# Kernel optimization log

Hardware: AMD Instinct MI355X
Metric: run time of the kernel (lower is better)

## Reference

```python
import jax, jax.numpy as jnp
import numpy as np

M = 0.25      # margin m
GAMMA = 64.0  # scale gamma
N, D = 8192, 128
NUM_CLASSES = 512


def setup_inputs() -> dict:
    key = jax.random.key(0)
    k1, k2 = jax.random.split(key)
    inputs = jax.random.normal(k1, (N, D), dtype=jnp.float32)
    targets = jax.random.randint(k2, (N,), 0, NUM_CLASSES, dtype=jnp.int64)
    return {"inputs": inputs, "targets": targets}


def reference(inputs, targets):
    # L2-normalize rows -> cosine similarity matrix [n, n]
    x = inputs / jnp.linalg.norm(inputs, axis=1, keepdims=True)
    sim = x @ x.T
    # positive mask: same label (includes diagonal, matching the torch code)
    mask = targets[:, None] == targets[None, :]

    Op, On = 1.0 + M, -M
    delta_p, delta_n = 1.0 - M, M

    sim_d = jax.lax.stop_gradient(sim)  # .detach() in torch
    ap = jnp.maximum(Op - sim_d, 0.0)
    an = jnp.maximum(sim_d + On, 0.0)

    logit_p = -ap * (sim - delta_p) * GAMMA
    logit_n = an * (sim - delta_n) * GAMMA

    neg_inf = jnp.float32(-jnp.inf)
    # per-row logsumexp over positives of -logit_p, over negatives of logit_n
    lp = jax.nn.logsumexp(jnp.where(mask, -logit_p, neg_inf), axis=1)
    ln = jax.nn.logsumexp(jnp.where(mask, neg_inf, logit_n), axis=1)

    return jnp.mean(jax.nn.softplus(ln + lp))
```

## Files before the change

### kernel.cpp

```cpp
#include <hip/hip_runtime.h>
#include <math.h>


#define NR    8192
#define DIMK  128
#define NT    64
#define NBLKS 512

typedef __attribute__((ext_vector_type(8))) short short8;
typedef __attribute__((ext_vector_type(4))) float f32x4;
typedef __attribute__((address_space(3))) uint32_t lds_u32;
typedef const __attribute__((address_space(1))) uint32_t glb_u32;

__device__ __forceinline__ unsigned short bf16_rne(float f) {
  uint32_t u = __float_as_uint(f);
  u += 0x7FFFu + ((u >> 16) & 1u);
  return (unsigned short)(u >> 16);
}


__global__ __launch_bounds__(256) void normalize_split_kernel(
    const float* __restrict__ x, unsigned short* __restrict__ xhi,
    unsigned short* __restrict__ xlo, float* __restrict__ gP,
    float* __restrict__ gN, int* __restrict__ counter) {
  if (blockIdx.x < 32)      gP[blockIdx.x * 256 + threadIdx.x] = 0.f;
  else if (blockIdx.x < 64) gN[(blockIdx.x - 32) * 256 + threadIdx.x] = 0.f;
  if (blockIdx.x == 64 && threadIdx.x == 0) *counter = 0;

  const int wave = threadIdx.x >> 6;
  const int lane = threadIdx.x & 63;
  const int row  = blockIdx.x * 4 + wave;
  const float2 v = ((const float2*)(x + (size_t)row * DIMK))[lane];
  float ss = v.x * v.x + v.y * v.y;
  #pragma unroll
  for (int s = 1; s < 64; s <<= 1) ss += __shfl_xor(ss, s);
  const float r = rsqrtf(ss);
  const float a = v.x * r, b = v.y * r;
  const unsigned short ha = bf16_rne(a), hb = bf16_rne(b);
  const float haf = __uint_as_float((uint32_t)ha << 16);
  const float hbf = __uint_as_float((uint32_t)hb << 16);
  ushort2 hi, lo;
  hi.x = ha; hi.y = hb;
  lo.x = bf16_rne(a - haf); lo.y = bf16_rne(b - hbf);
  ((ushort2*)xhi)[(size_t)row * 64 + lane] = hi;
  ((ushort2*)xlo)[(size_t)row * 64 + lane] = lo;
}

__global__ __launch_bounds__(512, 2) void simloss_kernel(
    const unsigned short* __restrict__ xhi, const unsigned short* __restrict__ xlo,
    const int* __restrict__ tgt, float* __restrict__ gP, float* __restrict__ gN,
    int* __restrict__ counter, float* __restrict__ out) {
  __shared__ unsigned short S[32768];
  __shared__ float colbuf[2][4][128][2];
  __shared__ int tAs[2][128];
  __shared__ int tBs[5][128];
  __shared__ float red[512];
  __shared__ int islast;

  const int tid  = threadIdx.x;
  const int wave = tid >> 6, lane = tid & 63;
  const int wy = wave & 3, wx = wave >> 2;
  const int q = lane >> 4, mcol = lane & 15;
  const bool isStage = (wy == 1) || (wy == 2);
  const bool isFlush = (wy == 0);
  const int srank = (wy - 1) + wx * 2;

  const int p  = blockIdx.x >> 4;
  const int b  = blockIdx.x & 15;
  const int n1 = NT - p;
  const int t0 = (b * (NT + 1)) >> 4;
  const int t1 = ((b + 1) * (NT + 1)) >> 4;
  const int ntile = t1 - t0;
  const int p2 = NT - 1 - p;

  int cur_bi = (t0 < n1) ? p : p2;

  if (tid < 128)       tAs[0][tid] = tgt[cur_bi * 128 + tid];
  else if (tid < 256)  tAs[1][tid - 128] = tgt[p2 * 128 + (tid - 128)];
  for (int v = tid; v < ntile * 128; v += 512) {
    const int ix = t0 + (v >> 7);
    const int bj = (ix < n1) ? p + ix : p2 + (ix - n1);
    tBs[v >> 7][v & 127] = tgt[bj * 128 + (v & 127)];
  }

  auto stageA = [&](int bi) {
    const unsigned short* gh = xhi + (size_t)bi * 128 * DIMK;
    const unsigned short* gl = xlo + (size_t)bi * 128 * DIMK;
    #pragma unroll
    for (int g = 0; g < 4; ++g) {
      const int r  = wave * 16 + g * 4 + (lane >> 4);
      const int sc = (lane & 15) ^ (r & 15);
      __builtin_amdgcn_global_load_lds((glb_u32*)(gh + (size_t)r * DIMK + sc * 8),
          (lds_u32*)&S[(wave * 16 + g * 4) * 128], 16, 0, 0);
      __builtin_amdgcn_global_load_lds((glb_u32*)(gl + (size_t)r * DIMK + sc * 8),
          (lds_u32*)&S[16384 + (wave * 16 + g * 4) * 128], 16, 0, 0);
    }
  };
  auto stageB = [&](int bj, int buf) {
    const unsigned short* gb = xhi + (size_t)bj * 128 * DIMK;
    unsigned short* dst = &S[buf * 16384];
    #pragma unroll
    for (int g = 0; g < 8; ++g) {
      const int r  = srank * 32 + g * 4 + (lane >> 4);
      const int sc = (lane & 15) ^ (r & 15);
      __builtin_amdgcn_global_load_lds((glb_u32*)(gb + (size_t)r * DIMK + sc * 8),
          (lds_u32*)&dst[(srank * 32 + g * 4) * 128], 16, 0, 0);
    }
  };

  short8 Ah[2][4], Al[2][4];
  int ta[2][4];
  auto extractA = [&](int seg) {
    #pragma unroll
    for (int fr = 0; fr < 2; ++fr) {
      const int r = wy * 32 + fr * 16 + mcol;
      #pragma unroll
      for (int ks = 0; ks < 4; ++ks) {
        const int pc = (ks * 4 + q) ^ mcol;
        Ah[fr][ks] = *(const short8*)&S[r * 128 + pc * 8];
        Al[fr][ks] = *(const short8*)&S[16384 + r * 128 + pc * 8];
      }
    }
    #pragma unroll
    for (int fr = 0; fr < 2; ++fr)
      #pragma unroll
      for (int rg = 0; rg < 4; ++rg)
        ta[fr][rg] = tAs[seg][wy * 32 + fr * 16 + q * 4 + rg];
  };

  float rowP[2][4] = {{0.f}}, rowN[2][4] = {{0.f}};
  auto flushRows = [&](int bi) {
    #pragma unroll
    for (int fr = 0; fr < 2; ++fr)
      #pragma unroll
      for (int rg = 0; rg < 4; ++rg) {
        float vp = rowP[fr][rg], vn = rowN[fr][rg];
        #pragma unroll
        for (int m = 1; m < 16; m <<= 1) {
          vp += __shfl_xor(vp, m);
          vn += __shfl_xor(vn, m);
        }
        if (mcol == 0) {
          const int row = bi * 128 + wy * 32 + fr * 16 + q * 4 + rg;
          atomicAdd(&gP[row], vp);
          atomicAdd(&gN[row], vn);
        }
      }
  };

  stageA(cur_bi);
  __syncthreads();
  extractA(0);
  __builtin_amdgcn_s_waitcnt(49279);
  __builtin_amdgcn_s_barrier();
  if (isStage) stageB((t0 < n1) ? p + t0 : p2 + (t0 - n1), 0);

  for (int tl = 0; tl < ntile; ++tl) {
    const int ix = t0 + tl;
    const int bi = (ix < n1) ? p : p2;
    const int bj = (ix < n1) ? p + ix : p2 + (ix - n1);

    if (bi != cur_bi) {
      flushRows(cur_bi);
      cur_bi = bi;
      stageA(cur_bi);
      __syncthreads();
      extractA(1);
      #pragma unroll
      for (int fr = 0; fr < 2; ++fr)
        #pragma unroll
        for (int rg = 0; rg < 4; ++rg) { rowP[fr][rg] = 0.f; rowN[fr][rg] = 0.f; }
      __builtin_amdgcn_s_waitcnt(49279);
      __builtin_amdgcn_s_barrier();
      if (isStage) stageB(bj, tl & 1);
    }

    if (isStage) __builtin_amdgcn_s_waitcnt(112);
    __builtin_amdgcn_s_barrier();

    if (tl + 1 < ntile) {
      const int ix2 = ix + 1;
      if ((ix2 < n1) == (ix < n1)) {
        const int bj2 = (ix2 < n1) ? p + ix2 : p2 + (ix2 - n1);
        if (isStage) stageB(bj2, (tl + 1) & 1);
      }
    }

    const unsigned short* Bb = &S[(tl & 1) * 16384];
    f32x4 acc[2][4];
    #pragma unroll
    for (int fr = 0; fr < 2; ++fr)
      #pragma unroll
      for (int fc = 0; fc < 4; ++fc)
        acc[fr][fc] = (f32x4){0.f, 0.f, 0.f, 0.f};
    #pragma unroll
    for (int ks = 0; ks < 4; ++ks) {
      short8 bh[4];
      #pragma unroll
      for (int fc = 0; fc < 4; ++fc) {
        const int rb = wx * 64 + fc * 16 + mcol;
        const int pc = (ks * 4 + q) ^ mcol;
        bh[fc] = *(const short8*)&Bb[rb * 128 + pc * 8];
      }
      #pragma unroll
      for (int fc = 0; fc < 4; ++fc) {
        acc[0][fc] = __builtin_amdgcn_mfma_f32_16x16x32_bf16(Ah[0][ks], bh[fc], acc[0][fc], 0, 0, 0);
        acc[1][fc] = __builtin_amdgcn_mfma_f32_16x16x32_bf16(Ah[1][ks], bh[fc], acc[1][fc], 0, 0, 0);
        acc[0][fc] = __builtin_amdgcn_mfma_f32_16x16x32_bf16(Al[0][ks], bh[fc], acc[0][fc], 0, 0, 0);
        acc[1][fc] = __builtin_amdgcn_mfma_f32_16x16x32_bf16(Al[1][ks], bh[fc], acc[1][fc], 0, 0, 0);
      }
    }

    int tb[4];
    #pragma unroll
    for (int fc = 0; fc < 4; ++fc) tb[fc] = tBs[tl][wx * 64 + fc * 16 + mcol];
    float cP[4] = {0.f, 0.f, 0.f, 0.f}, cN[4] = {0.f, 0.f, 0.f, 0.f};
    #pragma unroll
    for (int fr = 0; fr < 2; ++fr) {
      #pragma unroll
      for (int rg = 0; rg < 4; ++rg) {
        const int taa = ta[fr][rg];
        float vp = 0.f, vn = 0.f;
        #pragma unroll
        for (int fc = 0; fc < 4; ++fc) {
          const float s  = acc[fr][fc][rg];
          const bool pos = (taa == tb[fc]);
          const float ap = fmaxf(1.25f - s, 0.f);
          const float an = fmaxf(s - 0.25f, 0.f);
          const float arg = pos ? ap * fmaf(s, 64.f, -48.f) : an * an * 64.f;
          const float e = __expf(arg);
          const float ep = pos ? e : 0.f;
          const float en = pos ? 0.f : e;
          vp += ep; vn += en;
          cP[fc] += ep; cN[fc] += en;
        }
        rowP[fr][rg] += vp;
        rowN[fr][rg] += vn;
      }
    }

    #pragma unroll
    for (int fc = 0; fc < 4; ++fc) {
      cP[fc] += __shfl_xor(cP[fc], 16); cP[fc] += __shfl_xor(cP[fc], 32);
      cN[fc] += __shfl_xor(cN[fc], 16); cN[fc] += __shfl_xor(cN[fc], 32);
    }
    if (q == 0) {
      #pragma unroll
      for (int fc = 0; fc < 4; ++fc) {
        float2 v; v.x = cP[fc]; v.y = cN[fc];
        *(float2*)&colbuf[tl & 1][wy][wx * 64 + fc * 16 + mcol][0] = v;
      }
    }
    __builtin_amdgcn_s_waitcnt(49279);
    __builtin_amdgcn_s_barrier();

    if (isFlush && bj != bi) {
      const int col = wx * 64 + lane;
      float sp = 0.f, sn = 0.f;
      #pragma unroll
      for (int w = 0; w < 4; ++w) {
        const float2 v = *(const float2*)&colbuf[tl & 1][w][col][0];
        sp += v.x; sn += v.y;
      }
      atomicAdd(&gP[bj * 128 + col], sp);
      atomicAdd(&gN[bj * 128 + col], sn);
    }
  }
  flushRows(cur_bi);

  __builtin_amdgcn_s_waitcnt(0);
  __syncthreads();
  if (tid == 0) islast = (atomicAdd(counter, 1) == NBLKS - 1) ? 1 : 0;
  __syncthreads();
  if (islast) {
    float local = 0.f;
    #pragma unroll 1
    for (int bb = 0; bb < 2; ++bb) {
      const int base = bb * 4096 + tid * 8;
      float pv[8], nv[8];
      #pragma unroll
      for (int u = 0; u < 8; ++u) pv[u] = atomicAdd(&gP[base + u], 0.0f);
      #pragma unroll
      for (int u = 0; u < 8; ++u) nv[u] = atomicAdd(&gN[base + u], 0.0f);
      #pragma unroll
      for (int u = 0; u < 8; ++u) local += log1pf(pv[u] * nv[u]);
    }
    red[tid] = local;
    __syncthreads();
    for (int s2 = 256; s2 > 0; s2 >>= 1) {
      if (tid < s2) red[tid] += red[tid + s2];
      __syncthreads();
    }
    if (tid == 0) out[0] = red[0] / (float)NR;
  }
}

extern "C" void kernel_launch(void* const* d_in, const int* in_sizes, int n_in,
                              void* d_out, int out_size, void* d_ws, size_t ws_size,
                              hipStream_t stream) {
  const float* x  = (const float*)d_in[0];
  const int* tgt  = (const int*)d_in[1];
  float* out      = (float*)d_out;

  unsigned short* xhi = (unsigned short*)d_ws;
  unsigned short* xlo = xhi + (size_t)NR * DIMK;
  float* gP = (float*)((char*)d_ws + (size_t)NR * DIMK * 4);
  float* gN = gP + NR;
  int* counter = (int*)(gN + NR);

  normalize_split_kernel<<<NR / 4, 256, 0, stream>>>(x, xhi, xlo, gP, gN, counter);
  simloss_kernel<<<NBLKS, 512, 0, stream>>>(xhi, xlo, tgt, gP, gN, counter, out);
}
```

Baseline: 121.4 us.

## Drop LDS staging and load MFMA operands directly from global memory

Removes the LDS double-buffered staging of the A and B tiles, the target arrays and the column-reduction buffer. Each wave now reads its bf16 fragments and targets straight from global memory, relying on L1/L2 caching. This eliminates block-wide barriers and LDS traffic. The work split changes to 416 blocks of exactly 5 tiles each. Column partial sums are now atomically added per wave instead of being combined in LDS first. The trade-off is redundant global loads across waves, no explicit prefetch overlap, and four times more column atomics.

```diff
diff --git a/kernel.cpp b/kernel.cpp
--- a/kernel.cpp
+++ b/kernel.cpp
@@ -5,12 +5,10 @@
 #define NR    8192
 #define DIMK  128
 #define NT    64
-#define NBLKS 512
+#define NBLKS 416
 
 typedef __attribute__((ext_vector_type(8))) short short8;
 typedef __attribute__((ext_vector_type(4))) float f32x4;
-typedef __attribute__((address_space(3))) uint32_t lds_u32;
-typedef const __attribute__((address_space(1))) uint32_t glb_u32;
 
 __device__ __forceinline__ unsigned short bf16_rne(float f) {
   uint32_t u = __float_as_uint(f);
@@ -50,10 +48,6 @@
     const unsigned short* __restrict__ xhi, const unsigned short* __restrict__ xlo,
     const int* __restrict__ tgt, float* __restrict__ gP, float* __restrict__ gN,
     int* __restrict__ counter, float* __restrict__ out) {
-  __shared__ unsigned short S[32768];
-  __shared__ float colbuf[2][4][128][2];
-  __shared__ int tAs[2][128];
-  __shared__ int tBs[5][128];
   __shared__ float red[512];
   __shared__ int islast;
 
@@ -61,74 +55,39 @@
   const int wave = tid >> 6, lane = tid & 63;
   const int wy = wave & 3, wx = wave >> 2;
   const int q = lane >> 4, mcol = lane & 15;
-  const bool isStage = (wy == 1) || (wy == 2);
-  const bool isFlush = (wy == 0);
-  const int srank = (wy - 1) + wx * 2;
-
-  const int p  = blockIdx.x >> 4;
-  const int b  = blockIdx.x & 15;
+
+  const int p  = blockIdx.x / 13;
+  const int b  = blockIdx.x - p * 13;
   const int n1 = NT - p;
-  const int t0 = (b * (NT + 1)) >> 4;
-  const int t1 = ((b + 1) * (NT + 1)) >> 4;
-  const int ntile = t1 - t0;
   const int p2 = NT - 1 - p;
-
-  int cur_bi = (t0 < n1) ? p : p2;
-
-  if (tid < 128)       tAs[0][tid] = tgt[cur_bi * 128 + tid];
-  else if (tid < 256)  tAs[1][tid - 128] = tgt[p2 * 128 + (tid - 128)];
-  for (int v = tid; v < ntile * 128; v += 512) {
-    const int ix = t0 + (v >> 7);
-    const int bj = (ix < n1) ? p + ix : p2 + (ix - n1);
-    tBs[v >> 7][v & 127] = tgt[bj * 128 + (v & 127)];
-  }
-
-  auto stageA = [&](int bi) {
-    const unsigned short* gh = xhi + (size_t)bi * 128 * DIMK;
-    const unsigned short* gl = xlo + (size_t)bi * 128 * DIMK;
-    #pragma unroll
-    for (int g = 0; g < 4; ++g) {
-      const int r  = wave * 16 + g * 4 + (lane >> 4);
-      const int sc = (lane & 15) ^ (r & 15);
-      __builtin_amdgcn_global_load_lds((glb_u32*)(gh + (size_t)r * DIMK + sc * 8),
-          (lds_u32*)&S[(wave * 16 + g * 4) * 128], 16, 0, 0);
-      __builtin_amdgcn_global_load_lds((glb_u32*)(gl + (size_t)r * DIMK + sc * 8),
-          (lds_u32*)&S[16384 + (wave * 16 + g * 4) * 128], 16, 0, 0);
-    }
-  };
-  auto stageB = [&](int bj, int buf) {
-    const unsigned short* gb = xhi + (size_t)bj * 128 * DIMK;
-    unsigned short* dst = &S[buf * 16384];
-    #pragma unroll
-    for (int g = 0; g < 8; ++g) {
-      const int r  = srank * 32 + g * 4 + (lane >> 4);
-      const int sc = (lane & 15) ^ (r & 15);
-      __builtin_amdgcn_global_load_lds((glb_u32*)(gb + (size_t)r * DIMK + sc * 8),
-          (lds_u32*)&dst[(srank * 32 + g * 4) * 128], 16, 0, 0);
-    }
-  };
+  const int t0 = b * 5;
 
   short8 Ah[2][4], Al[2][4];
   int ta[2][4];
-  auto extractA = [&](int seg) {
+  float rowP[2][4], rowN[2][4];
+
+  auto loadA = [&](int bi) {
     #pragma unroll
     for (int fr = 0; fr < 2; ++fr) {
-      const int r = wy * 32 + fr * 16 + mcol;
+      const int r = bi * 128 + wy * 32 + fr * 16 + mcol;
+      const unsigned short* gh = xhi + (size_t)r * DIMK + q * 8;
+      const unsigned short* gl = xlo + (size_t)r * DIMK + q * 8;
       #pragma unroll
       for (int ks = 0; ks < 4; ++ks) {
-        const int pc = (ks * 4 + q) ^ mcol;
-        Ah[fr][ks] = *(const short8*)&S[r * 128 + pc * 8];
-        Al[fr][ks] = *(const short8*)&S[16384 + r * 128 + pc * 8];
-      }
-    }
+        Ah[fr][ks] = *(const short8*)(gh + ks * 32);
+        Al[fr][ks] = *(const short8*)(gl + ks * 32);
+      }
+      #pragma unroll
+      for (int rg = 0; rg < 4; ++rg)
+        ta[fr][rg] = tgt[bi * 128 + wy * 32 + fr * 16 + q * 4 + rg];
+    }
+  };
+  auto zeroRows = [&]() {
     #pragma unroll
     for (int fr = 0; fr < 2; ++fr)
       #pragma unroll
-      for (int rg = 0; rg < 4; ++rg)
-        ta[fr][rg] = tAs[seg][wy * 32 + fr * 16 + q * 4 + rg];
+      for (int rg = 0; rg < 4; ++rg) { rowP[fr][rg] = 0.f; rowN[fr][rg] = 0.f; }
   };
-
-  float rowP[2][4] = {{0.f}}, rowN[2][4] = {{0.f}};
   auto flushRows = [&](int bi) {
     #pragma unroll
     for (int fr = 0; fr < 2; ++fr)
@@ -148,59 +107,36 @@
       }
   };
 
-  stageA(cur_bi);
-  __syncthreads();
-  extractA(0);
-  __builtin_amdgcn_s_waitcnt(49279);
-  __builtin_amdgcn_s_barrier();
-  if (isStage) stageB((t0 < n1) ? p + t0 : p2 + (t0 - n1), 0);
-
-  for (int tl = 0; tl < ntile; ++tl) {
+  int cur_bi = (t0 < n1) ? p : p2;
+  loadA(cur_bi);
+  zeroRows();
+
+  for (int tl = 0; tl < 5; ++tl) {
     const int ix = t0 + tl;
     const int bi = (ix < n1) ? p : p2;
     const int bj = (ix < n1) ? p + ix : p2 + (ix - n1);
 
     if (bi != cur_bi) {
       flushRows(cur_bi);
+      zeroRows();
       cur_bi = bi;
-      stageA(cur_bi);
-      __syncthreads();
-      extractA(1);
-      #pragma unroll
-      for (int fr = 0; fr < 2; ++fr)
-        #pragma unroll
-        for (int rg = 0; rg < 4; ++rg) { rowP[fr][rg] = 0.f; rowN[fr][rg] = 0.f; }
-      __builtin_amdgcn_s_waitcnt(49279);
-      __builtin_amdgcn_s_barrier();
-      if (isStage) stageB(bj, tl & 1);
-    }
-
-    if (isStage) __builtin_amdgcn_s_waitcnt(112);
-    __builtin_amdgcn_s_barrier();
-
-    if (tl + 1 < ntile) {
-      const int ix2 = ix + 1;
-      if ((ix2 < n1) == (ix < n1)) {
-        const int bj2 = (ix2 < n1) ? p + ix2 : p2 + (ix2 - n1);
-        if (isStage) stageB(bj2, (tl + 1) & 1);
-      }
-    }
-
-    const unsigned short* Bb = &S[(tl & 1) * 16384];
+      loadA(bi);
+    }
+
     f32x4 acc[2][4];
     #pragma unroll
     for (int fr = 0; fr < 2; ++fr)
       #pragma unroll
       for (int fc = 0; fc < 4; ++fc)
         acc[fr][fc] = (f32x4){0.f, 0.f, 0.f, 0.f};
+
     #pragma unroll
     for (int ks = 0; ks < 4; ++ks) {
       short8 bh[4];
       #pragma unroll
       for (int fc = 0; fc < 4; ++fc) {
-        const int rb = wx * 64 + fc * 16 + mcol;
-        const int pc = (ks * 4 + q) ^ mcol;
-        bh[fc] = *(const short8*)&Bb[rb * 128 + pc * 8];
+        const int rb = bj * 128 + wx * 64 + fc * 16 + mcol;
+        bh[fc] = *(const short8*)(xhi + (size_t)rb * DIMK + ks * 32 + q * 8);
       }
       #pragma unroll
       for (int fc = 0; fc < 4; ++fc) {
@@ -213,7 +149,9 @@
 
     int tb[4];
     #pragma unroll
-    for (int fc = 0; fc < 4; ++fc) tb[fc] = tBs[tl][wx * 64 + fc * 16 + mcol];
+    for (int fc = 0; fc < 4; ++fc)
+      tb[fc] = tgt[bj * 128 + wx * 64 + fc * 16 + mcol];
+
     float cP[4] = {0.f, 0.f, 0.f, 0.f}, cN[4] = {0.f, 0.f, 0.f, 0.f};
     #pragma unroll
     for (int fr = 0; fr < 2; ++fr) {
@@ -239,31 +177,18 @@
       }
     }
 
-    #pragma unroll
-    for (int fc = 0; fc < 4; ++fc) {
-      cP[fc] += __shfl_xor(cP[fc], 16); cP[fc] += __shfl_xor(cP[fc], 32);
-      cN[fc] += __shfl_xor(cN[fc], 16); cN[fc] += __shfl_xor(cN[fc], 32);
-    }
-    if (q == 0) {
+    if (bj != bi) {
       #pragma unroll
       for (int fc = 0; fc < 4; ++fc) {
-        float2 v; v.x = cP[fc]; v.y = cN[fc];
-        *(float2*)&colbuf[tl & 1][wy][wx * 64 + fc * 16 + mcol][0] = v;
-      }
-    }
-    __builtin_amdgcn_s_waitcnt(49279);
-    __builtin_amdgcn_s_barrier();
-
-    if (isFlush && bj != bi) {
-      const int col = wx * 64 + lane;
-      float sp = 0.f, sn = 0.f;
-      #pragma unroll
-      for (int w = 0; w < 4; ++w) {
-        const float2 v = *(const float2*)&colbuf[tl & 1][w][col][0];
-        sp += v.x; sn += v.y;
-      }
-      atomicAdd(&gP[bj * 128 + col], sp);
-      atomicAdd(&gN[bj * 128 + col], sn);
+        float a = cP[fc], bb = cN[fc];
+        a  += __shfl_xor(a, 16);  a  += __shfl_xor(a, 32);
+        bb += __shfl_xor(bb, 16); bb += __shfl_xor(bb, 32);
+        if (q == 0) {
+          const int col = bj * 128 + wx * 64 + fc * 16 + mcol;
+          atomicAdd(&gP[col], a);
+          atomicAdd(&gN[col], bb);
+        }
+      }
     }
   }
   flushRows(cur_bi);
```

New measurement: 134.2 us. +10.5%, slower.
